# Kernel tuning notes

Measured on AMD Instinct MI355X. Metric: run time of the kernel, lower is better.

The kernel has to match this reference:

```python
import jax, jax.numpy as jnp
import numpy as np

B, Q, S, D, H = 8, 100, 4096, 256, 8
HD = D // H
EPS = 1e-5


def layer_norm(x, g, b):
    mu = jnp.mean(x, axis=-1, keepdims=True)
    var = jnp.mean(jnp.square(x - mu), axis=-1, keepdims=True)
    return (x - mu) * jax.lax.rsqrt(var + EPS) * g + b


def mha(q_in, k_in, v_in, w_in, b_in, w_out, b_out, bias=None):
    # torch nn.MultiheadAttention math (batch_first, dropout=0)
    wq, wk, wv = jnp.split(w_in, 3, axis=0)
    bq, bk, bv = jnp.split(b_in, 3, axis=0)
    Bq, Lq, _ = q_in.shape
    Lk = k_in.shape[1]
    q = (q_in @ wq.T + bq).reshape(Bq, Lq, H, HD)
    k = (k_in @ wk.T + bk).reshape(Bq, Lk, H, HD)
    v = (v_in @ wv.T + bv).reshape(Bq, Lk, H, HD)
    scores = jnp.einsum('bqhd,bkhd->bhqk', q, k) / jnp.sqrt(jnp.asarray(HD, q.dtype))
    if bias is not None:
        scores = scores + bias  # [B,1,Q,S] broadcast over heads (same per head)
    attn = jax.nn.softmax(scores, axis=-1)
    out = jnp.einsum('bhqk,bkhd->bqhd', attn, v).reshape(Bq, Lq, D)
    return out @ w_out.T + b_out


def setup_inputs() -> dict:
    key = jax.random.key(0)
    ks = jax.random.split(key, 12)
    s = 0.02
    return {
        'queries': jax.random.normal(ks[0], (B, Q, D), jnp.float32),
        'pixel_feat': jax.random.normal(ks[1], (B, S, D), jnp.float32),
        'prev_mask': jax.random.normal(ks[2], (B, Q, S), jnp.float32),
        'cross_in_w': jax.random.normal(ks[3], (3 * D, D), jnp.float32) * s,
        'cross_in_b': jnp.zeros((3 * D,), jnp.float32),
        'cross_out_w': jax.random.normal(ks[4], (D, D), jnp.float32) * s,
        'cross_out_b': jnp.zeros((D,), jnp.float32),
        'self_in_w': jax.random.normal(ks[5], (3 * D, D), jnp.float32) * s,
        'self_in_b': jnp.zeros((3 * D,), jnp.float32),
        'self_out_w': jax.random.normal(ks[6], (D, D), jnp.float32) * s,
        'self_out_b': jnp.zeros((D,), jnp.float32),
        'ln_cross_g': jnp.ones((D,), jnp.float32),
        'ln_cross_b': jnp.zeros((D,), jnp.float32),
        'ln_self_g': jnp.ones((D,), jnp.float32),
        'ln_self_b': jnp.zeros((D,), jnp.float32),
        'ln_ffn_g': jnp.ones((D,), jnp.float32),
        'ln_ffn_b': jnp.zeros((D,), jnp.float32),
        'ffn_w1': jax.random.normal(ks[7], (4 * D, D), jnp.float32) * s,
        'ffn_b1': jnp.zeros((4 * D,), jnp.float32),
        'ffn_w2': jax.random.normal(ks[8], (D, 4 * D), jnp.float32) * s,
        'ffn_b2': jnp.zeros((D,), jnp.float32),
    }


def reference(queries, pixel_feat, prev_mask,
              cross_in_w, cross_in_b, cross_out_w, cross_out_b,
              self_in_w, self_in_b, self_out_w, self_out_b,
              ln_cross_g, ln_cross_b, ln_self_g, ln_self_b, ln_ffn_g, ln_ffn_b,
              ffn_w1, ffn_b1, ffn_w2, ffn_b2):
    # masked cross-attn bias (no-grad region in torch; boolean ops have no grad)
    region = jax.nn.sigmoid(prev_mask) > 0.5                    # [B,Q,S]
    any_pos = jnp.any(region, axis=-1, keepdims=True)
    region = jnp.where(any_pos, region, jnp.ones_like(region))
    bias = (~region).astype(queries.dtype) * -10000.0
    bias = bias[:, None, :, :]                                  # [B,1,Q,S]

    q_out = mha(layer_norm(queries, ln_cross_g, ln_cross_b), pixel_feat, pixel_feat,
                cross_in_w, cross_in_b, cross_out_w, cross_out_b, bias)
    queries = queries + q_out

    q_norm = layer_norm(queries, ln_self_g, ln_self_b)
    q_out = mha(q_norm, q_norm, q_norm, self_in_w, self_in_b, self_out_w, self_out_b)
    queries = queries + q_out

    h = layer_norm(queries, ln_ffn_g, ln_ffn_b)
    h = jax.nn.gelu(h @ ffn_w1.T + ffn_b1, approximate=False) @ ffn_w2.T + ffn_b2
    return queries + h
```

## Files before the change

### kernel.cpp

```cpp
#include <hip/hip_runtime.h>
#include <hip/hip_bf16.h>
#include <math.h>

#define BQ 100
#define SB 8
#define SS 4096
#define DD 256
#define HH 8
#define HDD 32
#define NSPLIT 4
#define SCHUNK (SS / NSPLIT)
#define MROWS 800

typedef __attribute__((ext_vector_type(8))) short bf16x8;
typedef __attribute__((ext_vector_type(4))) float f32x4;

__device__ inline unsigned short f2bf(float f) {
    union { float f; unsigned u; } v; v.f = f;
    unsigned r = v.u + 0x7fff + ((v.u >> 16) & 1);
    return (unsigned short)(r >> 16);
}

__device__ inline unsigned pkbf(float x, float y) {
    union { __hip_bfloat162 h; unsigned u; } c;
    c.h = __float22bfloat162_rn(make_float2(x, y));
    return c.u;
}

__device__ inline bf16x8 load_bf8(const float* p) {
    float4 a = *(const float4*)p;
    float4 b = *(const float4*)(p + 4);
    union { unsigned u[4]; bf16x8 v; } r;
    r.u[0] = pkbf(a.x, a.y); r.u[1] = pkbf(a.z, a.w);
    r.u[2] = pkbf(b.x, b.y); r.u[3] = pkbf(b.z, b.w);
    return r.v;
}

#define TM 128
#define TN 128
#define TK 32
#define LSTR 40

#define WOFF_CW   0
#define WOFF_SIW  196608
#define WOFF_COW  393216
#define WOFF_SOW  458752
#define WOFF_F1   524288
#define WOFF_F2   786432
#define WTOT      1048576

__global__ __launch_bounds__(256) void wprep(
        const float* __restrict__ cw, const float* __restrict__ siw,
        const float* __restrict__ cow, const float* __restrict__ sow,
        const float* __restrict__ f1, const float* __restrict__ f2,
        unsigned short* __restrict__ o) {
    int b = blockIdx.x;
    const float* src; size_t so, doff;
    if (b < 96)       { src = cw;  so = (size_t)b * 2048;         doff = WOFF_CW; }
    else if (b < 192) { src = siw; so = (size_t)(b - 96) * 2048;  doff = WOFF_SIW; }
    else if (b < 224) { src = cow; so = (size_t)(b - 192) * 2048; doff = WOFF_COW; }
    else if (b < 256) { src = sow; so = (size_t)(b - 224) * 2048; doff = WOFF_SOW; }
    else if (b < 384) { src = f1;  so = (size_t)(b - 256) * 2048; doff = WOFF_F1; }
    else              { src = f2;  so = (size_t)(b - 384) * 2048; doff = WOFF_F2; }
    int t = threadIdx.x;
    const float* p = src + so + (size_t)t * 8;
    float4 a = *(const float4*)p;
    float4 c = *(const float4*)(p + 4);
    uint4 pk;
    pk.x = pkbf(a.x, a.y); pk.y = pkbf(a.z, a.w);
    pk.z = pkbf(c.x, c.y); pk.w = pkbf(c.z, c.w);
    *(uint4*)(o + doff + so + (size_t)t * 8) = pk;
}

__global__ __launch_bounds__(256, 4) void stage1(
        const float* __restrict__ queries,
        const float* __restrict__ ln_g, const float* __restrict__ ln_b,
        const unsigned short* __restrict__ wbf,
        const float* __restrict__ cb,
        float* __restrict__ q_cross,
        const float* __restrict__ pixel_feat,
        unsigned short* __restrict__ Kb, unsigned short* __restrict__ Vb,
        const float* __restrict__ mask, unsigned* __restrict__ Mbits) {
    __shared__ __align__(16) char smem[21504];
    const int bid = blockIdx.x;
    const int t = threadIdx.x;

    if (bid < 1024) {
        typedef unsigned short (*tile_t)[LSTR];
        tile_t As = (tile_t)smem;
        const float* A = pixel_feat;
        const unsigned short* Wb = wbf + (size_t)DD * DD;
        const float* bias = cb + DD;
        int xcd = bid & 7, idx = bid >> 3;
        int mt = xcd + 8 * (idx >> 2);
        int ntl = idx & 3;
        int m0 = mt * TM, n0 = ntl * TN;
        int wave = t / 64, lane = t % 64;
        int wm = (wave % 2) * 64, wn = (wave / 2) * 64;
        int lr = t / 4, lc = (t % 4) * 8;
        int fr = lane % 16, quad = lane / 16;
        f32x4 acc[4][4] = {};

        const float* Arow0 = A + (size_t)(m0 + lr) * DD + lc;
        const float* Arow1 = A + (size_t)(m0 + lr + 64) * DD + lc;
        const unsigned short* Wfr = Wb + (size_t)(n0 + wn + fr) * DD + quad * 8;

        float4 p00 = *(const float4*)(Arow0);
        float4 p01 = *(const float4*)(Arow0 + 4);
        float4 p10 = *(const float4*)(Arow1);
        float4 p11 = *(const float4*)(Arow1 + 4);

        for (int k0 = 0; k0 < DD; k0 += TK) {
            __syncthreads();
            uint4 pk0, pk1;
            pk0.x = pkbf(p00.x, p00.y); pk0.y = pkbf(p00.z, p00.w);
            pk0.z = pkbf(p01.x, p01.y); pk0.w = pkbf(p01.z, p01.w);
            *(uint4*)&As[lr][lc] = pk0;
            pk1.x = pkbf(p10.x, p10.y); pk1.y = pkbf(p10.z, p10.w);
            pk1.z = pkbf(p11.x, p11.y); pk1.w = pkbf(p11.z, p11.w);
            *(uint4*)&As[lr + 64][lc] = pk1;
            if (k0 < DD - TK) {
                p00 = *(const float4*)(Arow0 + k0 + 32);
                p01 = *(const float4*)(Arow0 + k0 + 36);
                p10 = *(const float4*)(Arow1 + k0 + 32);
                p11 = *(const float4*)(Arow1 + k0 + 36);
            }
            bf16x8 bv0 = *(const bf16x8*)(Wfr + k0);
            bf16x8 bv1 = *(const bf16x8*)(Wfr + (size_t)16 * DD + k0);
            bf16x8 bv2 = *(const bf16x8*)(Wfr + (size_t)32 * DD + k0);
            bf16x8 bv3 = *(const bf16x8*)(Wfr + (size_t)48 * DD + k0);
            __syncthreads();
            bf16x8 af[4];
#pragma unroll
            for (int mi = 0; mi < 4; mi++)
                af[mi] = *(const bf16x8*)&As[wm + mi * 16 + fr][quad * 8];
#pragma unroll
            for (int mi = 0; mi < 4; mi++) {
                acc[mi][0] = __builtin_amdgcn_mfma_f32_16x16x32_bf16(af[mi], bv0, acc[mi][0], 0, 0, 0);
                acc[mi][1] = __builtin_amdgcn_mfma_f32_16x16x32_bf16(af[mi], bv1, acc[mi][1], 0, 0, 0);
                acc[mi][2] = __builtin_amdgcn_mfma_f32_16x16x32_bf16(af[mi], bv2, acc[mi][2], 0, 0, 0);
                acc[mi][3] = __builtin_amdgcn_mfma_f32_16x16x32_bf16(af[mi], bv3, acc[mi][3], 0, 0, 0);
            }
        }
#pragma unroll
        for (int ni = 0; ni < 4; ni++) {
            int n = n0 + wn + ni * 16 + fr;
            float bv = bias[n];
            unsigned short* dst = (n < 256) ? Kb : Vb;
            int hh = (n >> 5) & 7, d = n & 31;
#pragma unroll
            for (int mi = 0; mi < 4; mi++) {
#pragma unroll
                for (int r = 0; r < 4; r++) {
                    int m = m0 + wm + mi * 16 + quad * 4 + r;
                    int bb = m >> 12, s = m & (SS - 1);
                    dst[((((size_t)bb * HH + hh) * SS + s) << 5) + d] =
                        f2bf(acc[mi][ni][r] + bv);
                }
            }
        }
    } else if (bid < 1824) {
        int row = bid - 1024;
        unsigned* words = (unsigned*)smem;
        unsigned* orred = (unsigned*)(smem + 512);
        int w = t >> 6, lane = t & 63;
        const float* mp = mask + (size_t)row * SS + lane;
        float mv[16];
#pragma unroll
        for (int i = 0; i < 16; i++) mv[i] = mp[(w * 16 + i) * 64];
        unsigned lor = 0;
#pragma unroll
        for (int i = 0; i < 16; i++) {
            unsigned long long bal = __ballot(mv[i] > 0.f);
            if (lane == 0) {
                words[(w * 16 + i) * 2] = (unsigned)bal;
                words[(w * 16 + i) * 2 + 1] = (unsigned)(bal >> 32);
            }
            lor |= (unsigned)(bal | (bal >> 32));
        }
        if (lane == 0) orred[w] = lor;
        __syncthreads();
        unsigned anyv = orred[0] | orred[1] | orred[2] | orred[3];
        if (t < 128) Mbits[(size_t)row * 128 + t] = anyv ? words[t] : 0xFFFFFFFFu;
    } else {
        typedef unsigned short (*arow_t)[264];
        arow_t Aq = (arow_t)smem;
        float* mu_s = (float*)(smem + 16896);
        float* rs_s = mu_s + 32;
        float (*prt)[8][2] = (float(*)[8][2])(rs_s + 32);
        int idx = bid - 1824;
        int nq = idx & 1, my = idx >> 1;
        int m0 = my * 32;
        int row = t & 31, cs = t >> 5;
        const float* xp = queries + (size_t)(m0 + row) * DD + cs * 32;
        float s = 0.f, ss = 0.f;
#pragma unroll
        for (int c = 0; c < 32; c += 4) {
            float4 v = *(const float4*)(xp + c);
            s += v.x + v.y + v.z + v.w;
            ss += v.x * v.x + v.y * v.y + v.z * v.z + v.w * v.w;
        }
        prt[row][cs][0] = s; prt[row][cs][1] = ss;
        __syncthreads();
        if (t < 32) {
            float sum = 0.f, sq = 0.f;
#pragma unroll
            for (int k = 0; k < 8; k++) { sum += prt[t][k][0]; sq += prt[t][k][1]; }
            float mu = sum * (1.0f / DD);
            float var = sq * (1.0f / DD) - mu * mu;
            mu_s[t] = mu;
            rs_s[t] = rsqrtf(var + 1e-5f);
        }
        __syncthreads();
        {
            float mu = mu_s[row], r = rs_s[row];
            int col0 = cs * 32;
#pragma unroll
            for (int c = 0; c < 32; c += 8) {
                int col = col0 + c;
                float4 v0 = *(const float4*)(xp + c);
                float4 v1 = *(const float4*)(xp + c + 4);
                float4 g0 = *(const float4*)(ln_g + col);
                float4 g1 = *(const float4*)(ln_g + col + 4);
                float4 b0 = *(const float4*)(ln_b + col);
                float4 b1 = *(const float4*)(ln_b + col + 4);
                uint4 pk;
                pk.x = pkbf((v0.x - mu) * r * g0.x + b0.x, (v0.y - mu) * r * g0.y + b0.y);
                pk.y = pkbf((v0.z - mu) * r * g0.z + b0.z, (v0.w - mu) * r * g0.w + b0.w);
                pk.z = pkbf((v1.x - mu) * r * g1.x + b1.x, (v1.y - mu) * r * g1.y + b1.y);
                pk.w = pkbf((v1.z - mu) * r * g1.z + b1.z, (v1.w - mu) * r * g1.w + b1.w);
                *(uint4*)&Aq[row][col] = pk;
            }
        }
        __syncthreads();
        int w = t >> 6, lane = t & 63;
        int fr = lane & 15, quad = lane >> 4;
        int n0 = nq * 128 + w * 32;
        f32x4 acc[2][2] = {};
        const unsigned short* Wq0 = wbf + (size_t)(n0 + fr) * DD + quad * 8;
        const unsigned short* Wq1 = Wq0 + (size_t)16 * DD;
#pragma unroll
        for (int k0 = 0; k0 < DD; k0 += 32) {
            bf16x8 a0 = *(const bf16x8*)&Aq[fr][k0 + quad * 8];
            bf16x8 a1 = *(const bf16x8*)&Aq[16 + fr][k0 + quad * 8];
            bf16x8 w0 = *(const bf16x8*)(Wq0 + k0);
            bf16x8 w1 = *(const bf16x8*)(Wq1 + k0);
            acc[0][0] = __builtin_amdgcn_mfma_f32_16x16x32_bf16(a0, w0, acc[0][0], 0, 0, 0);
            acc[0][1] = __builtin_amdgcn_mfma_f32_16x16x32_bf16(a0, w1, acc[0][1], 0, 0, 0);
            acc[1][0] = __builtin_amdgcn_mfma_f32_16x16x32_bf16(a1, w0, acc[1][0], 0, 0, 0);
            acc[1][1] = __builtin_amdgcn_mfma_f32_16x16x32_bf16(a1, w1, acc[1][1], 0, 0, 0);
        }
#pragma unroll
        for (int ni = 0; ni < 2; ni++) {
            int n = n0 + ni * 16 + fr;
            float bv = cb[n];
#pragma unroll
            for (int mi = 0; mi < 2; mi++) {
#pragma unroll
                for (int r = 0; r < 4; r++) {
                    int m = m0 + mi * 16 + quad * 4 + r;
                    q_cross[(size_t)m * DD + n] = acc[mi][ni][r] + bv;
                }
            }
        }
    }
}

template<int MODE>
__global__ __launch_bounds__(64, 4) void ln_gemm(
        const float* __restrict__ X, const float* __restrict__ gam,
        const float* __restrict__ bet,
        const unsigned short* __restrict__ W, const float* __restrict__ bias,
        const float* __restrict__ res,
        float* __restrict__ C, int N) {
    __shared__ unsigned short As[32][264];
    __shared__ float mu_s[32], rs_s[32];
    __shared__ float prt[32][2][2];
    const int t = threadIdx.x;
    const int fr = t & 15, quad = t >> 4;
    const int m0 = blockIdx.y * 32, n0 = blockIdx.x * 32;
    const int row = t & 31, half = t >> 5;

    const float* xp = X + (size_t)(m0 + row) * DD + half * 128;
    float s = 0.f, ss = 0.f;
#pragma unroll
    for (int c = 0; c < 128; c += 4) {
        float4 v = *(const float4*)(xp + c);
        s += v.x + v.y + v.z + v.w;
        ss += v.x * v.x + v.y * v.y + v.z * v.z + v.w * v.w;
    }
    prt[row][half][0] = s;
    prt[row][half][1] = ss;
    __syncthreads();
    if (t < 32) {
        float sum = prt[t][0][0] + prt[t][1][0];
        float sq  = prt[t][0][1] + prt[t][1][1];
        float mu = sum * (1.0f / DD);
        float var = sq * (1.0f / DD) - mu * mu;
        mu_s[t] = mu;
        rs_s[t] = rsqrtf(var + 1e-5f);
    }
    __syncthreads();
    {
        float mu = mu_s[row], r = rs_s[row];
#pragma unroll
        for (int c = 0; c < 128; c += 8) {
            int col = half * 128 + c;
            float4 v0 = *(const float4*)(xp + c);
            float4 v1 = *(const float4*)(xp + c + 4);
            float4 g0 = *(const float4*)(gam + col);
            float4 g1 = *(const float4*)(gam + col + 4);
            float4 b0 = *(const float4*)(bet + col);
            float4 b1 = *(const float4*)(bet + col + 4);
            uint4 pk;
            pk.x = pkbf((v0.x - mu) * r * g0.x + b0.x, (v0.y - mu) * r * g0.y + b0.y);
            pk.y = pkbf((v0.z - mu) * r * g0.z + b0.z, (v0.w - mu) * r * g0.w + b0.w);
            pk.z = pkbf((v1.x - mu) * r * g1.x + b1.x, (v1.y - mu) * r * g1.y + b1.y);
            pk.w = pkbf((v1.z - mu) * r * g1.z + b1.z, (v1.w - mu) * r * g1.w + b1.w);
            *(uint4*)&As[row][col] = pk;
        }
    }
    __syncthreads();

    f32x4 acc[2][2] = {};
    const unsigned short* Wp0 = W + (size_t)(n0 + fr) * DD + quad * 8;
    const unsigned short* Wp1 = Wp0 + (size_t)16 * DD;
#pragma unroll
    for (int k0 = 0; k0 < DD; k0 += 32) {
        bf16x8 a0 = *(const bf16x8*)&As[fr][k0 + quad * 8];
        bf16x8 a1 = *(const bf16x8*)&As[16 + fr][k0 + quad * 8];
        bf16x8 w0 = *(const bf16x8*)(Wp0 + k0);
        bf16x8 w1 = *(const bf16x8*)(Wp1 + k0);
        acc[0][0] = __builtin_amdgcn_mfma_f32_16x16x32_bf16(a0, w0, acc[0][0], 0, 0, 0);
        acc[0][1] = __builtin_amdgcn_mfma_f32_16x16x32_bf16(a0, w1, acc[0][1], 0, 0, 0);
        acc[1][0] = __builtin_amdgcn_mfma_f32_16x16x32_bf16(a1, w0, acc[1][0], 0, 0, 0);
        acc[1][1] = __builtin_amdgcn_mfma_f32_16x16x32_bf16(a1, w1, acc[1][1], 0, 0, 0);
    }

#pragma unroll
    for (int ni = 0; ni < 2; ni++) {
        int n = n0 + ni * 16 + fr;
        float bv = bias[n];
#pragma unroll
        for (int mi = 0; mi < 2; mi++) {
#pragma unroll
            for (int r = 0; r < 4; r++) {
                int m = m0 + mi * 16 + quad * 4 + r;
                float v = acc[mi][ni][r] + bv;
                if (MODE == 1) {
                    v = 0.5f * v * (1.0f + erff(v * 0.70710678118654752f));
                } else if (MODE == 2) {
                    v += res[(size_t)m * N + n];
                }
                C[(size_t)m * N + n] = v;
            }
        }
    }
}

__global__ __launch_bounds__(64, 4) void comb_gemm(
        const float* __restrict__ Opart, const float* __restrict__ mpart,
        const float* __restrict__ lpart,
        const unsigned short* __restrict__ W, const float* __restrict__ bias,
        const float* __restrict__ res,
        float* __restrict__ C) {
    __shared__ unsigned short As[32][264];
    const int t = threadIdx.x;
    const int fr = t & 15, quad = t >> 4;
    const int m0 = blockIdx.y * 32, n0 = blockIdx.x * 32;
    const int row = t & 31, half = t >> 5;

    {
        int m = m0 + row;
        int b = m / BQ, q = m % BQ;
#pragma unroll
        for (int h = half * 4; h < half * 4 + 4; h++) {
            float mv[NSPLIT], wsp[NSPLIT];
            float mstar = -1e30f;
#pragma unroll
            for (int sp = 0; sp < NSPLIT; sp++) {
                mv[sp] = mpart[((size_t)(b * NSPLIT + sp) * HH + h) * BQ + q];
                mstar = fmaxf(mstar, mv[sp]);
            }
            float lstar = 0.f;
#pragma unroll
            for (int sp = 0; sp < NSPLIT; sp++) {
                wsp[sp] = __expf(mv[sp] - mstar);
                lstar += lpart[((size_t)(b * NSPLIT + sp) * HH + h) * BQ + q] * wsp[sp];
            }
            float inv = 1.0f / lstar;
#pragma unroll
            for (int d = 0; d < HDD; d += 8) {
                float o[8] = {};
#pragma unroll
                for (int sp = 0; sp < NSPLIT; sp++) {
                    const float* op = Opart +
                        ((size_t)(b * NSPLIT + sp) * BQ + q) * DD + h * HDD + d;
                    float4 a = *(const float4*)op;
                    float4 b4 = *(const float4*)(op + 4);
                    o[0] += a.x * wsp[sp];  o[1] += a.y * wsp[sp];
                    o[2] += a.z * wsp[sp];  o[3] += a.w * wsp[sp];
                    o[4] += b4.x * wsp[sp]; o[5] += b4.y * wsp[sp];
                    o[6] += b4.z * wsp[sp]; o[7] += b4.w * wsp[sp];
                }
                uint4 pk;
                pk.x = pkbf(o[0] * inv, o[1] * inv);
                pk.y = pkbf(o[2] * inv, o[3] * inv);
                pk.z = pkbf(o[4] * inv, o[5] * inv);
                pk.w = pkbf(o[6] * inv, o[7] * inv);
                *(uint4*)&As[row][h * HDD + d] = pk;
            }
        }
    }
    __syncthreads();

    f32x4 acc[2][2] = {};
    const unsigned short* Wp0 = W + (size_t)(n0 + fr) * DD + quad * 8;
    const unsigned short* Wp1 = Wp0 + (size_t)16 * DD;
#pragma unroll
    for (int k0 = 0; k0 < DD; k0 += 32) {
        bf16x8 a0 = *(const bf16x8*)&As[fr][k0 + quad * 8];
        bf16x8 a1 = *(const bf16x8*)&As[16 + fr][k0 + quad * 8];
        bf16x8 w0 = *(const bf16x8*)(Wp0 + k0);
        bf16x8 w1 = *(const bf16x8*)(Wp1 + k0);
        acc[0][0] = __builtin_amdgcn_mfma_f32_16x16x32_bf16(a0, w0, acc[0][0], 0, 0, 0);
        acc[0][1] = __builtin_amdgcn_mfma_f32_16x16x32_bf16(a0, w1, acc[0][1], 0, 0, 0);
        acc[1][0] = __builtin_amdgcn_mfma_f32_16x16x32_bf16(a1, w0, acc[1][0], 0, 0, 0);
        acc[1][1] = __builtin_amdgcn_mfma_f32_16x16x32_bf16(a1, w1, acc[1][1], 0, 0, 0);
    }

#pragma unroll
    for (int ni = 0; ni < 2; ni++) {
        int n = n0 + ni * 16 + fr;
        float bv = bias[n];
#pragma unroll
        for (int mi = 0; mi < 2; mi++) {
#pragma unroll
            for (int r = 0; r < 4; r++) {
                int m = m0 + mi * 16 + quad * 4 + r;
                float v = acc[mi][ni][r] + bv + res[(size_t)m * DD + n];
                C[(size_t)m * DD + n] = v;
            }
        }
    }
}

template<int KK, int SPLITK, int MODE>
__global__ __launch_bounds__(64, 4) void gemm_skinny2(
        const float* __restrict__ A, const unsigned short* __restrict__ W,
        const float* __restrict__ bias, const float* __restrict__ res,
        float* __restrict__ C, float* __restrict__ Cp, int N) {
    const int lane = threadIdx.x;
    const int fr = lane & 15, quad = lane >> 4;
    const int m0 = blockIdx.y * 32;
    const int n0 = blockIdx.x * 32;
    const int sk = blockIdx.z;
    const int KCH = KK / SPLITK;

    f32x4 acc[2][2] = {};
    const float* Ap0 = A + (size_t)(m0 + fr) * KK + sk * KCH + quad * 8;
    const float* Ap1 = Ap0 + (size_t)16 * KK;
    const unsigned short* Wp0 = W + (size_t)(n0 + fr) * KK + sk * KCH + quad * 8;
    const unsigned short* Wp1 = Wp0 + (size_t)16 * KK;

#pragma unroll
    for (int k0 = 0; k0 < KCH; k0 += 32) {
        bf16x8 a0 = load_bf8(Ap0 + k0);
        bf16x8 a1 = load_bf8(Ap1 + k0);
        bf16x8 w0 = *(const bf16x8*)(Wp0 + k0);
        bf16x8 w1 = *(const bf16x8*)(Wp1 + k0);
        acc[0][0] = __builtin_amdgcn_mfma_f32_16x16x32_bf16(a0, w0, acc[0][0], 0, 0, 0);
        acc[0][1] = __builtin_amdgcn_mfma_f32_16x16x32_bf16(a0, w1, acc[0][1], 0, 0, 0);
        acc[1][0] = __builtin_amdgcn_mfma_f32_16x16x32_bf16(a1, w0, acc[1][0], 0, 0, 0);
        acc[1][1] = __builtin_amdgcn_mfma_f32_16x16x32_bf16(a1, w1, acc[1][1], 0, 0, 0);
    }

    if (SPLITK == 1) {
#pragma unroll
        for (int ni = 0; ni < 2; ni++) {
            int n = n0 + ni * 16 + fr;
            float bv = bias[n];
#pragma unroll
            for (int mi = 0; mi < 2; mi++) {
#pragma unroll
                for (int r = 0; r < 4; r++) {
                    int m = m0 + mi * 16 + quad * 4 + r;
                    float v = acc[mi][ni][r] + bv;
                    if (MODE == 1) {
                        v = 0.5f * v * (1.0f + erff(v * 0.70710678118654752f));
                    } else if (MODE == 2) {
                        v += res[(size_t)m * N + n];
                    }
                    C[(size_t)m * N + n] = v;
                }
            }
        }
    } else {
        float* dst = Cp + (size_t)sk * MROWS * N;
#pragma unroll
        for (int ni = 0; ni < 2; ni++) {
            int n = n0 + ni * 16 + fr;
#pragma unroll
            for (int mi = 0; mi < 2; mi++) {
#pragma unroll
                for (int r = 0; r < 4; r++) {
                    int m = m0 + mi * 16 + quad * 4 + r;
                    dst[(size_t)m * N + n] = acc[mi][ni][r];
                }
            }
        }
    }
}

template<int SPLITK, int MODE>
__global__ void gemm_combine(const float* __restrict__ Cp,
                             const float* __restrict__ bias,
                             const float* __restrict__ res,
                             float* __restrict__ C, int N) {
    int m = blockIdx.x;
    for (int n = threadIdx.x; n < N; n += 256) {
        float v = bias[n];
#pragma unroll
        for (int sk = 0; sk < SPLITK; sk++)
            v += Cp[((size_t)sk * MROWS + m) * N + n];
        if (MODE == 1) {
            v = 0.5f * v * (1.0f + erff(v * 0.70710678118654752f));
        } else if (MODE == 2) {
            v += res[(size_t)m * N + n];
        }
        C[(size_t)m * N + n] = v;
    }
}

#define QT 64
#define ST 128

__global__ __launch_bounds__(256) void cross_attn_mfma(
        const float* __restrict__ Qm,
        const unsigned short* __restrict__ Kb,
        const unsigned short* __restrict__ Vb,
        const unsigned* __restrict__ Mbits,
        float* __restrict__ Opart,
        float* __restrict__ mpart,
        float* __restrict__ lpart) {
    __shared__ unsigned short Qs[QT][40];
    __shared__ unsigned short Ks[ST][40];
    __shared__ unsigned short Vt[HDD][136];
    __shared__ unsigned short Ps[QT][136];
    __shared__ unsigned Mq[QT][4];
    __shared__ float red[QT][17];
    __shared__ float m_s[QT], alpha_s[QT], l_s[QT];

    const int qb = blockIdx.x, h = blockIdx.y;
    const int b = blockIdx.z / NSPLIT, sp = blockIdx.z % NSPLIT;
    const int t = threadIdx.x;
    const int w = t >> 6, lane = t & 63;
    const int fr = lane & 15, quad = lane >> 4;
    const int q0 = qb * QT;
    const int qlim = min(BQ - q0, QT);

    {
        int q = t >> 2, c0 = (t & 3) * 8;
        float4 v0 = make_float4(0.f, 0.f, 0.f, 0.f), v1 = v0;
        if (q < qlim) {
            const float* qp = Qm + (size_t)(b * BQ + q0 + q) * DD + h * HDD + c0;
            v0 = *(const float4*)qp;
            v1 = *(const float4*)(qp + 4);
        }
        const float sc = 0.17677669529663687f;
        uint4 pq;
        pq.x = pkbf(v0.x * sc, v0.y * sc);
        pq.y = pkbf(v0.z * sc, v0.w * sc);
        pq.z = pkbf(v1.x * sc, v1.y * sc);
        pq.w = pkbf(v1.z * sc, v1.w * sc);
        *(uint4*)&Qs[q][c0] = pq;
        if (t < QT) { m_s[t] = -1e30f; l_s[t] = 0.f; }
    }

    f32x4 oacc[2] = {};
    const unsigned short* Kbase = Kb + (((size_t)(b * HH + h)) * SS << 5);
    const unsigned short* Vbase = Vb + (((size_t)(b * HH + h)) * SS << 5);

    for (int s0 = sp * SCHUNK; s0 < (sp + 1) * SCHUNK; s0 += ST) {
        __syncthreads();
        {
            int r = t >> 1, half = t & 1;
            const unsigned short* kp = Kbase + ((size_t)(s0 + r) << 5) + half * 16;
            *(uint4*)&Ks[r][half * 16] = *(const uint4*)kp;
            *(uint4*)&Ks[r][half * 16 + 8] = *(const uint4*)(kp + 8);
            const unsigned short* vp = Vbase + ((size_t)(s0 + r) << 5) + half * 16;
            union { uint4 u; unsigned short s[8]; } v0, v1;
            v0.u = *(const uint4*)vp;
            v1.u = *(const uint4*)(vp + 8);
#pragma unroll
            for (int j = 0; j < 8; j++) Vt[half * 16 + j][r] = v0.s[j];
#pragma unroll
            for (int j = 0; j < 8; j++) Vt[half * 16 + 8 + j][r] = v1.s[j];
        }
        {
            int q = t >> 2, wd = t & 3;
            unsigned mword = 0xFFFFFFFFu;
            if (q < qlim)
                mword = Mbits[(size_t)(b * BQ + q0 + q) * 128 + (s0 >> 5) + wd];
            Mq[q][wd] = mword;
        }
        __syncthreads();

        bf16x8 af[2];
#pragma unroll
        for (int mt = 0; mt < 2; mt++)
            af[mt] = *(const bf16x8*)&Ks[w * 32 + mt * 16 + fr][quad * 8];
        f32x4 st[2][4];
#pragma unroll
        for (int nt = 0; nt < 4; nt++) {
            bf16x8 bq = *(const bf16x8*)&Qs[nt * 16 + fr][quad * 8];
#pragma unroll
            for (int mt = 0; mt < 2; mt++) {
                f32x4 z = {0.f, 0.f, 0.f, 0.f};
                st[mt][nt] = __builtin_amdgcn_mfma_f32_16x16x32_bf16(af[mt], bq, z, 0, 0, 0);
            }
        }

        float pmax[4] = {-1e30f, -1e30f, -1e30f, -1e30f};
#pragma unroll
        for (int nt = 0; nt < 4; nt++) {
            unsigned mword = Mq[nt * 16 + fr][w];
#pragma unroll
            for (int mt = 0; mt < 2; mt++)
#pragma unroll
                for (int r = 0; r < 4; r++) {
                    int bitpos = mt * 16 + quad * 4 + r;
                    float v = st[mt][nt][r];
                    if (!((mword >> bitpos) & 1u)) v -= 10000.f;
                    st[mt][nt][r] = v;
                    pmax[nt] = fmaxf(pmax[nt], v);
                }
        }
#pragma unroll
        for (int nt = 0; nt < 4; nt++)
            red[nt * 16 + fr][w * 4 + quad] = pmax[nt];
        __syncthreads();

        if (t < QT) {
            float mt_ = -1e30f;
#pragma unroll
            for (int k = 0; k < 16; k++) mt_ = fmaxf(mt_, red[t][k]);
            float mo = m_s[t], mn = fmaxf(mo, mt_);
            m_s[t] = mn;
            alpha_s[t] = __expf(mo - mn);
        }
        __syncthreads();

        float psum[4] = {0.f, 0.f, 0.f, 0.f};
#pragma unroll
        for (int nt = 0; nt < 4; nt++) {
            float mrow = m_s[nt * 16 + fr];
#pragma unroll
            for (int mt = 0; mt < 2; mt++) {
                float p0 = __expf(st[mt][nt][0] - mrow);
                float p1 = __expf(st[mt][nt][1] - mrow);
                float p2 = __expf(st[mt][nt][2] - mrow);
                float p3 = __expf(st[mt][nt][3] - mrow);
                psum[nt] += p0 + p1 + p2 + p3;
                uint2 pk;
                pk.x = pkbf(p0, p1);
                pk.y = pkbf(p2, p3);
                *(uint2*)&Ps[nt * 16 + fr][w * 32 + mt * 16 + quad * 4] = pk;
            }
        }
#pragma unroll
        for (int nt = 0; nt < 4; nt++)
            red[nt * 16 + fr][w * 4 + quad] = psum[nt];
        __syncthreads();

        if (t < QT) {
            float s = 0.f;
#pragma unroll
            for (int k = 0; k < 16; k++) s += red[t][k];
            l_s[t] = l_s[t] * alpha_s[t] + s;
        }

#pragma unroll
        for (int r = 0; r < 4; r++) {
            float a = alpha_s[w * 16 + quad * 4 + r];
            oacc[0][r] *= a; oacc[1][r] *= a;
        }
#pragma unroll
        for (int k0 = 0; k0 < ST; k0 += 32) {
            bf16x8 ap = *(const bf16x8*)&Ps[w * 16 + fr][k0 + quad * 8];
            bf16x8 bv0 = *(const bf16x8*)&Vt[fr][k0 + quad * 8];
            bf16x8 bv1 = *(const bf16x8*)&Vt[16 + fr][k0 + quad * 8];
            oacc[0] = __builtin_amdgcn_mfma_f32_16x16x32_bf16(ap, bv0, oacc[0], 0, 0, 0);
            oacc[1] = __builtin_amdgcn_mfma_f32_16x16x32_bf16(ap, bv1, oacc[1], 0, 0, 0);
        }
    }
    __syncthreads();

    int part = b * NSPLIT + sp;
    if (t < qlim) {
        mpart[((size_t)part * HH + h) * BQ + q0 + t] = m_s[t];
        lpart[((size_t)part * HH + h) * BQ + q0 + t] = l_s[t];
    }
#pragma unroll
    for (int nd = 0; nd < 2; nd++) {
#pragma unroll
        for (int r = 0; r < 4; r++) {
            int q = w * 16 + quad * 4 + r;
            if (q < qlim)
                Opart[((size_t)part * BQ + q0 + q) * DD + h * HDD + nd * 16 + fr] = oacc[nd][r];
        }
    }
}

__global__ void attn_kernel(const float* __restrict__ Qm, int sq, int qo0,
                            const float* __restrict__ Km, int sk, int ko0,
                            const float* __restrict__ Vm, int sv, int vo0,
                            float* __restrict__ Out, int so, int oo0,
                            int Slen, int Qlen, float scale) {
    int q = blockIdx.x, h = blockIdx.y, b = blockIdx.z;
    int tid = threadIdx.x;
    __shared__ float qv[32];
    __shared__ float sc[128];
    __shared__ float red[256];
    __shared__ float part[8][33];
    int qrow = b * Qlen + q;
    if (tid < 32) qv[tid] = Qm[(size_t)qrow * sq + qo0 + h * HDD + tid] * scale;
    __syncthreads();

    float lmax = -1e30f;
    for (int s = tid; s < Slen; s += 256) {
        const float* kp = Km + (size_t)(b * Slen + s) * sk + ko0 + h * HDD;
        float dot = 0.f;
#pragma unroll
        for (int d = 0; d < HDD; d += 4) {
            float4 k4 = *(const float4*)(kp + d);
            dot += qv[d] * k4.x + qv[d + 1] * k4.y + qv[d + 2] * k4.z + qv[d + 3] * k4.w;
        }
        sc[s] = dot;
        lmax = fmaxf(lmax, dot);
    }
    red[tid] = lmax; __syncthreads();
    for (int off = 128; off > 0; off >>= 1) {
        if (tid < off) red[tid] = fmaxf(red[tid], red[tid + off]);
        __syncthreads();
    }
    float m = red[0];
    __syncthreads();
    float lsum = 0.f;
    for (int s = tid; s < Slen; s += 256) {
        float e = __expf(sc[s] - m);
        sc[s] = e;
        lsum += e;
    }
    red[tid] = lsum; __syncthreads();
    for (int off = 128; off > 0; off >>= 1) {
        if (tid < off) red[tid] += red[tid + off];
        __syncthreads();
    }
    float inv = 1.0f / red[0];

    int d = tid & 31, g = tid >> 5;
    float acc = 0.f;
    for (int s = g; s < Slen; s += 8)
        acc += sc[s] * Vm[(size_t)(b * Slen + s) * sv + vo0 + h * HDD + d];
    part[g][d] = acc; __syncthreads();
    if (g == 0) {
        float t = 0.f;
#pragma unroll
        for (int gg = 0; gg < 8; gg++) t += part[gg][d];
        Out[(size_t)qrow * so + oo0 + h * HDD + d] = t * inv;
    }
}

extern "C" void kernel_launch(void* const* d_in, const int* in_sizes, int n_in,
                              void* d_out, int out_size, void* d_ws, size_t ws_size,
                              hipStream_t stream) {
    const float* queries    = (const float*)d_in[0];
    const float* pixel_feat = (const float*)d_in[1];
    const float* prev_mask  = (const float*)d_in[2];
    const float* cross_in_w  = (const float*)d_in[3];
    const float* cross_in_b  = (const float*)d_in[4];
    const float* cross_out_w = (const float*)d_in[5];
    const float* cross_out_b = (const float*)d_in[6];
    const float* self_in_w   = (const float*)d_in[7];
    const float* self_in_b   = (const float*)d_in[8];
    const float* self_out_w  = (const float*)d_in[9];
    const float* self_out_b  = (const float*)d_in[10];
    const float* ln_cross_g  = (const float*)d_in[11];
    const float* ln_cross_b  = (const float*)d_in[12];
    const float* ln_self_g   = (const float*)d_in[13];
    const float* ln_self_b   = (const float*)d_in[14];
    const float* ln_ffn_g    = (const float*)d_in[15];
    const float* ln_ffn_b    = (const float*)d_in[16];
    const float* ffn_w1 = (const float*)d_in[17];
    const float* ffn_b1 = (const float*)d_in[18];
    const float* ffn_w2 = (const float*)d_in[19];
    const float* ffn_b2 = (const float*)d_in[20];
    float* out = (float*)d_out;

    const int NQ = SB * BQ;
    const int NK = SB * SS;

    float* ws = (float*)d_ws;
    unsigned* Mbits = (unsigned*)ws;   ws += (size_t)NQ * 128;
    float* q_cross  = ws;              ws += (size_t)NQ * DD;
    unsigned short* Kbk = (unsigned short*)ws;
    ws += (size_t)NK * DD / 2;
    unsigned short* Vbk = (unsigned short*)ws;
    ws += (size_t)NK * DD / 2;
    float* queries1 = ws;              ws += (size_t)NQ * DD;
    float* qkv      = ws;              ws += (size_t)NQ * 3 * DD;
    float* attn2    = ws;              ws += (size_t)NQ * DD;
    float* queries2 = ws;              ws += (size_t)NQ * DD;
    float* ffn_h    = ws;              ws += (size_t)NQ * 4 * DD;
    float* Csplit   = ws;              ws += (size_t)4 * MROWS * DD;
    float* Opart    = ws;              ws += (size_t)SB * NSPLIT * BQ * DD;
    float* mpart    = ws;              ws += (size_t)SB * NSPLIT * HH * BQ;
    float* lpart    = ws;              ws += (size_t)SB * NSPLIT * HH * BQ;
    unsigned short* wbf = (unsigned short*)ws;

    const float scale = 0.17677669529663687f;

    wprep<<<512, 256, 0, stream>>>(
        cross_in_w, self_in_w, cross_out_w, self_out_w, ffn_w1, ffn_w2, wbf);

    stage1<<<1874, 256, 0, stream>>>(
        queries, ln_cross_g, ln_cross_b, wbf, cross_in_b, q_cross,
        pixel_feat, Kbk, Vbk, prev_mask, Mbits);

    cross_attn_mfma<<<dim3(2, HH, SB * NSPLIT), 256, 0, stream>>>(
        q_cross, Kbk, Vbk, Mbits, Opart, mpart, lpart);
    comb_gemm<<<dim3(8, 25), 64, 0, stream>>>(
        Opart, mpart, lpart, wbf + WOFF_COW, cross_out_b, queries, queries1);

    ln_gemm<0><<<dim3(24, 25), 64, 0, stream>>>(
        queries1, ln_self_g, ln_self_b, wbf + WOFF_SIW, self_in_b, nullptr,
        qkv, 3 * DD);
    attn_kernel<<<dim3(BQ, HH, SB), 256, 0, stream>>>(
        qkv, 3 * DD, 0, qkv, 3 * DD, DD, qkv, 3 * DD, 2 * DD,
        attn2, DD, 0, BQ, BQ, scale);
    gemm_skinny2<256, 1, 2><<<dim3(8, 25), 64, 0, stream>>>(
        attn2, wbf + WOFF_SOW, self_out_b, queries1, queries2, nullptr, DD);

    ln_gemm<1><<<dim3(32, 25), 64, 0, stream>>>(
        queries2, ln_ffn_g, ln_ffn_b, wbf + WOFF_F1, ffn_b1, nullptr,
        ffn_h, 4 * DD);
    gemm_skinny2<1024, 4, 2><<<dim3(8, 25, 4), 64, 0, stream>>>(
        ffn_h, wbf + WOFF_F2, ffn_b2, nullptr, nullptr, Csplit, DD);
    gemm_combine<4, 2><<<MROWS, 256, 0, stream>>>(
        Csplit, ffn_b2, queries2, out, DD);
}
```

Measured before the change: 253.4 us.

## Pre-convert pixel features to bf16 and load GEMM A fragments directly from global

The wprep kernel now also converts pixel_feat (8x4096x256 fp32) to bf16 in an extra workspace buffer using 4096 added blocks. The stage1 K/V projection GEMM then reads bf16 A fragments straight from global memory into registers, dropping the LDS staging, the in-loop fp32-to-bf16 packing and both __syncthreads per k-step, and fully unrolls the k loop. The cost is an extra full pass writing and re-reading a 16 MB bf16 copy, plus uncoalesced-ish per-lane fragment loads of A that each wave fetches without LDS sharing across waves.

```diff
diff --git a/kernel.cpp b/kernel.cpp
--- a/kernel.cpp
+++ b/kernel.cpp
@@ -39,7 +39,6 @@
 #define TM 128
 #define TN 128
 #define TK 32
-#define LSTR 40
 
 #define WOFF_CW   0
 #define WOFF_SIW  196608
@@ -53,8 +52,21 @@
         const float* __restrict__ cw, const float* __restrict__ siw,
         const float* __restrict__ cow, const float* __restrict__ sow,
         const float* __restrict__ f1, const float* __restrict__ f2,
-        unsigned short* __restrict__ o) {
+        const float* __restrict__ pix,
+        unsigned short* __restrict__ o, unsigned short* __restrict__ abf) {
     int b = blockIdx.x;
+    int t = threadIdx.x;
+    if (b >= 512) {
+        size_t off = (size_t)(b - 512) * 2048 + (size_t)t * 8;
+        const float* p = pix + off;
+        float4 a = *(const float4*)p;
+        float4 c = *(const float4*)(p + 4);
+        uint4 pk;
+        pk.x = pkbf(a.x, a.y); pk.y = pkbf(a.z, a.w);
+        pk.z = pkbf(c.x, c.y); pk.w = pkbf(c.z, c.w);
+        *(uint4*)(abf + off) = pk;
+        return;
+    }
     const float* src; size_t so, doff;
     if (b < 96)       { src = cw;  so = (size_t)b * 2048;         doff = WOFF_CW; }
     else if (b < 192) { src = siw; so = (size_t)(b - 96) * 2048;  doff = WOFF_SIW; }
@@ -62,7 +74,6 @@
     else if (b < 256) { src = sow; so = (size_t)(b - 224) * 2048; doff = WOFF_SOW; }
     else if (b < 384) { src = f1;  so = (size_t)(b - 256) * 2048; doff = WOFF_F1; }
     else              { src = f2;  so = (size_t)(b - 384) * 2048; doff = WOFF_F2; }
-    int t = threadIdx.x;
     const float* p = src + so + (size_t)t * 8;
     float4 a = *(const float4*)p;
     float4 c = *(const float4*)(p + 4);
@@ -78,7 +89,7 @@
         const unsigned short* __restrict__ wbf,
         const float* __restrict__ cb,
         float* __restrict__ q_cross,
-        const float* __restrict__ pixel_feat,
+        const unsigned short* __restrict__ Abf,
         unsigned short* __restrict__ Kb, unsigned short* __restrict__ Vb,
         const float* __restrict__ mask, unsigned* __restrict__ Mbits) {
     __shared__ __align__(16) char smem[21504];
@@ -86,9 +97,6 @@
     const int t = threadIdx.x;
 
     if (bid < 1024) {
-        typedef unsigned short (*tile_t)[LSTR];
-        tile_t As = (tile_t)smem;
-        const float* A = pixel_feat;
         const unsigned short* Wb = wbf + (size_t)DD * DD;
         const float* bias = cb + DD;
         int xcd = bid & 7, idx = bid >> 3;
@@ -97,49 +105,27 @@
         int m0 = mt * TM, n0 = ntl * TN;
         int wave = t / 64, lane = t % 64;
         int wm = (wave % 2) * 64, wn = (wave / 2) * 64;
-        int lr = t / 4, lc = (t % 4) * 8;
         int fr = lane % 16, quad = lane / 16;
         f32x4 acc[4][4] = {};
 
-        const float* Arow0 = A + (size_t)(m0 + lr) * DD + lc;
-        const float* Arow1 = A + (size_t)(m0 + lr + 64) * DD + lc;
-        const unsigned short* Wfr = Wb + (size_t)(n0 + wn + fr) * DD + quad * 8;
-
-        float4 p00 = *(const float4*)(Arow0);
-        float4 p01 = *(const float4*)(Arow0 + 4);
-        float4 p10 = *(const float4*)(Arow1);
-        float4 p11 = *(const float4*)(Arow1 + 4);
-
+        const unsigned short* Ap = Abf + (size_t)(m0 + wm + fr) * DD + quad * 8;
+        const unsigned short* Wp = Wb + (size_t)(n0 + wn + fr) * DD + quad * 8;
+
+#pragma unroll
         for (int k0 = 0; k0 < DD; k0 += TK) {
-            __syncthreads();
-            uint4 pk0, pk1;
-            pk0.x = pkbf(p00.x, p00.y); pk0.y = pkbf(p00.z, p00.w);
-            pk0.z = pkbf(p01.x, p01.y); pk0.w = pkbf(p01.z, p01.w);
-            *(uint4*)&As[lr][lc] = pk0;
-            pk1.x = pkbf(p10.x, p10.y); pk1.y = pkbf(p10.z, p10.w);
-            pk1.z = pkbf(p11.x, p11.y); pk1.w = pkbf(p11.z, p11.w);
-            *(uint4*)&As[lr + 64][lc] = pk1;
-            if (k0 < DD - TK) {
-                p00 = *(const float4*)(Arow0 + k0 + 32);
-                p01 = *(const float4*)(Arow0 + k0 + 36);
-                p10 = *(const float4*)(Arow1 + k0 + 32);
-                p11 = *(const float4*)(Arow1 + k0 + 36);
-            }
-            bf16x8 bv0 = *(const bf16x8*)(Wfr + k0);
-            bf16x8 bv1 = *(const bf16x8*)(Wfr + (size_t)16 * DD + k0);
-            bf16x8 bv2 = *(const bf16x8*)(Wfr + (size_t)32 * DD + k0);
-            bf16x8 bv3 = *(const bf16x8*)(Wfr + (size_t)48 * DD + k0);
-            __syncthreads();
-            bf16x8 af[4];
+            bf16x8 af[4], bv[4];
 #pragma unroll
             for (int mi = 0; mi < 4; mi++)
-                af[mi] = *(const bf16x8*)&As[wm + mi * 16 + fr][quad * 8];
+                af[mi] = *(const bf16x8*)(Ap + (size_t)mi * 16 * DD + k0);
+#pragma unroll
+            for (int ni = 0; ni < 4; ni++)
+                bv[ni] = *(const bf16x8*)(Wp + (size_t)ni * 16 * DD + k0);
 #pragma unroll
             for (int mi = 0; mi < 4; mi++) {
-                acc[mi][0] = __builtin_amdgcn_mfma_f32_16x16x32_bf16(af[mi], bv0, acc[mi][0], 0, 0, 0);
-                acc[mi][1] = __builtin_amdgcn_mfma_f32_16x16x32_bf16(af[mi], bv1, acc[mi][1], 0, 0, 0);
-                acc[mi][2] = __builtin_amdgcn_mfma_f32_16x16x32_bf16(af[mi], bv2, acc[mi][2], 0, 0, 0);
-                acc[mi][3] = __builtin_amdgcn_mfma_f32_16x16x32_bf16(af[mi], bv3, acc[mi][3], 0, 0, 0);
+                acc[mi][0] = __builtin_amdgcn_mfma_f32_16x16x32_bf16(af[mi], bv[0], acc[mi][0], 0, 0, 0);
+                acc[mi][1] = __builtin_amdgcn_mfma_f32_16x16x32_bf16(af[mi], bv[1], acc[mi][1], 0, 0, 0);
+                acc[mi][2] = __builtin_amdgcn_mfma_f32_16x16x32_bf16(af[mi], bv[2], acc[mi][2], 0, 0, 0);
+                acc[mi][3] = __builtin_amdgcn_mfma_f32_16x16x32_bf16(af[mi], bv[3], acc[mi][3], 0, 0, 0);
             }
         }
 #pragma unroll
@@ -818,15 +804,18 @@
     float* mpart    = ws;              ws += (size_t)SB * NSPLIT * HH * BQ;
     float* lpart    = ws;              ws += (size_t)SB * NSPLIT * HH * BQ;
     unsigned short* wbf = (unsigned short*)ws;
+    ws += WTOT / 2;
+    unsigned short* Abf = (unsigned short*)ws;
 
     const float scale = 0.17677669529663687f;
 
-    wprep<<<512, 256, 0, stream>>>(
-        cross_in_w, self_in_w, cross_out_w, self_out_w, ffn_w1, ffn_w2, wbf);
+    wprep<<<4608, 256, 0, stream>>>(
+        cross_in_w, self_in_w, cross_out_w, self_out_w, ffn_w1, ffn_w2,
+        pixel_feat, wbf, Abf);
 
     stage1<<<1874, 256, 0, stream>>>(
         queries, ln_cross_g, ln_cross_b, wbf, cross_in_b, q_cross,
-        pixel_feat, Kbk, Vbk, prev_mask, Mbits);
+        Abf, Kbk, Vbk, prev_mask, Mbits);
 
     cross_attn_mfma<<<dim3(2, HH, SB * NSPLIT), 256, 0, stream>>>(
         q_cross, Kbk, Vbk, Mbits, Opart, mpart, lpart);
```

New measurement: 273.2 us. +7.8%, slower.
